# Performance work log

Measured on AMD Instinct MI355X. Metric: run time of the kernel, lower is better.

The kernel has to match this reference:

```python
import jax, jax.numpy as jnp
import numpy as np

B, C, F, H = 8, 256, 128, 256  # batch, channels(nodes), bn_features, hidden_size


def setup_inputs() -> dict:
    key = jax.random.key(0)
    k1, k2, k3, k4 = jax.random.split(key, 4)
    s1 = 1.0 / np.sqrt(2 * F)  # torch Linear default init scale
    s2 = 1.0 / np.sqrt(H)
    return {
        "xa": jax.random.normal(k1, (B, C, F), dtype=jnp.float32),
        "W1": jax.random.uniform(k2, (H, 2 * F), jnp.float32, -s1, s1),
        "b1": jax.random.uniform(k3, (H,), jnp.float32, -s1, s1),
        "w2": jax.random.uniform(k4, (H,), jnp.float32, -s2, s2),
        "b2": jnp.zeros((), jnp.float32),
    }


def reference(xa, W1, b1, w2, b2):
    # Linear over cat([x_i, x_j]) == x_i @ Wa^T + x_j @ Wb^T  (split first layer;
    # identical math to torch's concat+Linear, avoids the (B,C,C,2F) concat).
    f = xa.shape[-1]
    Wa, Wb = W1[:, :f], W1[:, f:]
    a = jnp.einsum('bif,hf->bih', xa, Wa)          # (B,C,H)
    c = jnp.einsum('bjf,hf->bjh', xa, Wb)          # (B,C,H)
    h = jax.nn.relu(a[:, :, None, :] + c[:, None, :, :] + b1)  # (B,C,C,H)
    edge_logits = jnp.einsum('bijh,h->bij', h, w2) + b2         # (B,C,C)
    return jax.nn.sigmoid(edge_logits)
```

## Files before the change

kernel.cpp:

```cpp
#include <hip/hip_runtime.h>


typedef _Float16 h2 __attribute__((ext_vector_type(2)));
typedef _Float16 h8 __attribute__((ext_vector_type(8)));
typedef float    f4 __attribute__((ext_vector_type(4)));

constexpr int B  = 8;
constexpr int C  = 256;
constexpr int F  = 128;
constexpr int H  = 256;
constexpr int F2 = 2 * F;
constexpr int HOCT = H / 8;

#if __has_builtin(__builtin_amdgcn_fdot2)
__device__ __forceinline__ float fdot2(h2 a, h2 b, float c) {
    return __builtin_amdgcn_fdot2(a, b, c, false);
}
#else
__device__ __forceinline__ float fdot2(h2 a, h2 b, float c) {
    return c + (float)a.x * (float)b.x + (float)a.y * (float)b.y;
}
#endif

__device__ __forceinline__ h8 cvt8(float4 a, float4 b) {
    h8 r;
    r[0] = (_Float16)a.x; r[1] = (_Float16)a.y; r[2] = (_Float16)a.z; r[3] = (_Float16)a.w;
    r[4] = (_Float16)b.x; r[5] = (_Float16)b.y; r[6] = (_Float16)b.z; r[7] = (_Float16)b.w;
    return r;
}

__global__ __launch_bounds__(256) void k1_mfma(
    const float* __restrict__ xa, const float* __restrict__ W1,
    const float* __restrict__ b1, const float* __restrict__ w2,
    _Float16* __restrict__ Ah, _Float16* __restrict__ CP8,
    _Float16* __restrict__ w2h)
{
    const int t  = threadIdx.x;
    const int w  = blockIdx.x * 4 + (t >> 6);
    const int l  = t & 63;
    const int mg = w >> 4;
    const int h0 = (w & 15) * 16;
    const int lm = l & 15;
    const int lk = (l >> 4) * 8;
    const int m0 = mg * 32;

    h8 af[2][4];
    const float* xp0 = xa + (size_t)(m0 + lm) * F + lk;
    const float* xp1 = xp0 + 16 * F;
    #pragma unroll
    for (int kk = 0; kk < 4; ++kk) {
        float4 a0 = *(const float4*)(xp0 + kk * 32);
        float4 a1 = *(const float4*)(xp0 + kk * 32 + 4);
        float4 b0 = *(const float4*)(xp1 + kk * 32);
        float4 b1v = *(const float4*)(xp1 + kk * 32 + 4);
        af[0][kk] = cvt8(a0, a1);
        af[1][kk] = cvt8(b0, b1v);
    }

    const float* wp = W1 + (size_t)(h0 + lm) * F2 + lk;
    f4 accA0 = {0.f,0.f,0.f,0.f}, accA1 = {0.f,0.f,0.f,0.f};
    f4 accC0 = {0.f,0.f,0.f,0.f}, accC1 = {0.f,0.f,0.f,0.f};
    #pragma unroll
    for (int kk = 0; kk < 4; ++kk) {
        float4 wa0 = *(const float4*)(wp + kk * 32);
        float4 wa1 = *(const float4*)(wp + kk * 32 + 4);
        float4 wb0 = *(const float4*)(wp + F + kk * 32);
        float4 wb1 = *(const float4*)(wp + F + kk * 32 + 4);
        h8 ba = cvt8(wa0, wa1);
        h8 bb = cvt8(wb0, wb1);
        accA0 = __builtin_amdgcn_mfma_f32_16x16x32_f16(af[0][kk], ba, accA0, 0, 0, 0);
        accC0 = __builtin_amdgcn_mfma_f32_16x16x32_f16(af[0][kk], bb, accC0, 0, 0, 0);
        accA1 = __builtin_amdgcn_mfma_f32_16x16x32_f16(af[1][kk], ba, accA1, 0, 0, 0);
        accC1 = __builtin_amdgcn_mfma_f32_16x16x32_f16(af[1][kk], bb, accC1, 0, 0, 0);
    }

    const int h  = h0 + lm;
    const float bh = b1[h];
    #pragma unroll
    for (int mt = 0; mt < 2; ++mt) {
        const f4 aA = mt ? accA1 : accA0;
        const f4 aC = mt ? accC1 : accC0;
        const int mb = m0 + mt * 16 + (l >> 4) * 4;
        #pragma unroll
        for (int r = 0; r < 4; ++r) {
            const int m = mb + r;
            Ah[(size_t)m * H + h] = (_Float16)(aA[r] + bh);
            CP8[(((size_t)((m >> 8) * HOCT + (h >> 3)) * C + (m & 255)) << 3) + (h & 7)]
                = (_Float16)aC[r];
        }
    }

    if (blockIdx.x == 0 && t < 128) {
        float2 wv = ((const float2*)w2)[t];
        h2 hv = {(_Float16)wv.x, (_Float16)wv.y};
        ((h2*)w2h)[t] = hv;
    }
}

constexpr int TI = 8;
constexpr int HS = 4;

__global__ __launch_bounds__(1024) void k2_pair(
    const _Float16* __restrict__ Ah, const _Float16* __restrict__ CP8,
    const _Float16* __restrict__ w2h, const float* __restrict__ b2p,
    float* __restrict__ out)
{
    __shared__ float red[(HS - 1) * TI * C];
    const int t   = threadIdx.x;
    const int j   = t & 255;
    const int hs  = t >> 8;
    const int blk = blockIdx.x;
    const int it  = blk & 31;
    const int b   = blk >> 5;
    const int i0  = it * TI;

    float acc[TI];
    #pragma unroll
    for (int ii = 0; ii < TI; ++ii) acc[ii] = 0.f;

    const int g0 = hs * (HOCT / HS);
    const _Float16* Ab = Ah + (size_t)(b * C + i0) * H;

    union U { h8 v; h2 p[4]; };
    #pragma unroll 2
    for (int g = 0; g < HOCT / HS; ++g) {
        const int hb = g0 + g;
        h8 cc = *(const h8*)(CP8 + (((size_t)(b * HOCT + hb) * C + j) << 3));
        U uw; uw.v = *(const h8*)(w2h + hb * 8);
        #pragma unroll
        for (int ii = 0; ii < TI; ++ii) {
            h8 av = *(const h8*)(Ab + ii * H + hb * 8);
            h8 s = av + cc;
            h8 z = {0, 0, 0, 0, 0, 0, 0, 0};
            s = __builtin_elementwise_max(s, z);
            U us; us.v = s;
            float a0 = acc[ii];
            a0 = fdot2(us.p[0], uw.p[0], a0);
            a0 = fdot2(us.p[1], uw.p[1], a0);
            a0 = fdot2(us.p[2], uw.p[2], a0);
            a0 = fdot2(us.p[3], uw.p[3], a0);
            acc[ii] = a0;
        }
    }

    if (hs > 0) {
        #pragma unroll
        for (int ii = 0; ii < TI; ++ii)
            red[((hs - 1) * TI + ii) * C + j] = acc[ii];
    }
    __syncthreads();
    if (hs == 0) {
        const float bb = b2p[0];
        #pragma unroll
        for (int ii = 0; ii < TI; ++ii) {
            float x = acc[ii]
                    + red[(0 * TI + ii) * C + j]
                    + red[(1 * TI + ii) * C + j]
                    + red[(2 * TI + ii) * C + j] + bb;
            out[(size_t)(b * C + i0 + ii) * C + j] = 1.f / (1.f + __expf(-x));
        }
    }
}

extern "C" void kernel_launch(void* const* d_in, const int* in_sizes, int n_in,
                              void* d_out, int out_size, void* d_ws, size_t ws_size,
                              hipStream_t stream) {
    const float* xa = (const float*)d_in[0];
    const float* W1 = (const float*)d_in[1];
    const float* b1 = (const float*)d_in[2];
    const float* w2 = (const float*)d_in[3];
    const float* b2 = (const float*)d_in[4];
    float* out = (float*)d_out;

    _Float16* Ah  = (_Float16*)d_ws;
    _Float16* CP8 = Ah  + (size_t)B * C * H;
    _Float16* w2h = CP8 + (size_t)B * H * C;

    k1_mfma<<<256, 256, 0, stream>>>(xa, W1, b1, w2, Ah, CP8, w2h);
    k2_pair<<<B * (C / TI), 1024, 0, stream>>>(Ah, CP8, w2h, b2, out);
}
```

Baseline: 23.84 us.

## Fuse projection and pair kernels into one cooperative launch with grid sync

Merges the MFMA projection kernel and the pairwise edge kernel into a single cooperative kernel of 256 blocks by 1024 threads. The first 256 threads of each block do the projection, then a grid-wide sync separates the two phases. w2 is now converted to fp16 straight into registers instead of going through workspace memory, and the hidden loop is fully unrolled. This removes one launch and the gap between kernels, but adds grid-sync overhead, leaves 3/4 of the threads idle during phase one, and raises register pressure.

Result: slower. 62.35 us (+161.5%).

```diff
diff --git a/kernel.cpp b/kernel.cpp
--- a/kernel.cpp
+++ b/kernel.cpp
@@ -1,4 +1,7 @@
 #include <hip/hip_runtime.h>
+#include <hip/hip_cooperative_groups.h>
+
+namespace cg = cooperative_groups;
 
 
 typedef _Float16 h2 __attribute__((ext_vector_type(2)));
@@ -11,6 +14,8 @@
 constexpr int H  = 256;
 constexpr int F2 = 2 * F;
 constexpr int HOCT = H / 8;
+constexpr int TI = 8;
+constexpr int HS = 4;
 
 #if __has_builtin(__builtin_amdgcn_fdot2)
 __device__ __forceinline__ float fdot2(h2 a, h2 b, float c) {
@@ -29,90 +34,83 @@
     return r;
 }
 
-__global__ __launch_bounds__(256) void k1_mfma(
+__global__ __launch_bounds__(1024) void fused_kernel(
     const float* __restrict__ xa, const float* __restrict__ W1,
     const float* __restrict__ b1, const float* __restrict__ w2,
-    _Float16* __restrict__ Ah, _Float16* __restrict__ CP8,
-    _Float16* __restrict__ w2h)
+    const float* __restrict__ b2p, float* __restrict__ out,
+    _Float16* __restrict__ Ah, _Float16* __restrict__ CP8)
 {
-    const int t  = threadIdx.x;
-    const int w  = blockIdx.x * 4 + (t >> 6);
-    const int l  = t & 63;
-    const int mg = w >> 4;
-    const int h0 = (w & 15) * 16;
-    const int lm = l & 15;
-    const int lk = (l >> 4) * 8;
-    const int m0 = mg * 32;
+    __shared__ float red[(HS - 1) * TI * C];
+    const int t   = threadIdx.x;
+    const int blk = blockIdx.x;
 
-    h8 af[2][4];
-    const float* xp0 = xa + (size_t)(m0 + lm) * F + lk;
-    const float* xp1 = xp0 + 16 * F;
-    #pragma unroll
-    for (int kk = 0; kk < 4; ++kk) {
-        float4 a0 = *(const float4*)(xp0 + kk * 32);
-        float4 a1 = *(const float4*)(xp0 + kk * 32 + 4);
-        float4 b0 = *(const float4*)(xp1 + kk * 32);
-        float4 b1v = *(const float4*)(xp1 + kk * 32 + 4);
-        af[0][kk] = cvt8(a0, a1);
-        af[1][kk] = cvt8(b0, b1v);
-    }
+    if (t < 256) {
+        const int w  = blk * 4 + (t >> 6);
+        const int l  = t & 63;
+        const int mg = w >> 4;
+        const int h0 = (w & 15) * 16;
+        const int lm = l & 15;
+        const int lk = (l >> 4) * 8;
+        const int m0 = mg * 32;
 
-    const float* wp = W1 + (size_t)(h0 + lm) * F2 + lk;
-    f4 accA0 = {0.f,0.f,0.f,0.f}, accA1 = {0.f,0.f,0.f,0.f};
-    f4 accC0 = {0.f,0.f,0.f,0.f}, accC1 = {0.f,0.f,0.f,0.f};
-    #pragma unroll
-    for (int kk = 0; kk < 4; ++kk) {
-        float4 wa0 = *(const float4*)(wp + kk * 32);
-        float4 wa1 = *(const float4*)(wp + kk * 32 + 4);
-        float4 wb0 = *(const float4*)(wp + F + kk * 32);
-        float4 wb1 = *(const float4*)(wp + F + kk * 32 + 4);
-        h8 ba = cvt8(wa0, wa1);
-        h8 bb = cvt8(wb0, wb1);
-        accA0 = __builtin_amdgcn_mfma_f32_16x16x32_f16(af[0][kk], ba, accA0, 0, 0, 0);
-        accC0 = __builtin_amdgcn_mfma_f32_16x16x32_f16(af[0][kk], bb, accC0, 0, 0, 0);
-        accA1 = __builtin_amdgcn_mfma_f32_16x16x32_f16(af[1][kk], ba, accA1, 0, 0, 0);
-        accC1 = __builtin_amdgcn_mfma_f32_16x16x32_f16(af[1][kk], bb, accC1, 0, 0, 0);
-    }
+        h8 af[2][4];
+        const float* xp0 = xa + (size_t)(m0 + lm) * F + lk;
+        const float* xp1 = xp0 + 16 * F;
+        #pragma unroll
+        for (int kk = 0; kk < 4; ++kk) {
+            af[0][kk] = cvt8(*(const float4*)(xp0 + kk * 32),
+                             *(const float4*)(xp0 + kk * 32 + 4));
+            af[1][kk] = cvt8(*(const float4*)(xp1 + kk * 32),
+                             *(const float4*)(xp1 + kk * 32 + 4));
+        }
 
-    const int h  = h0 + lm;
-    const float bh = b1[h];
-    #pragma unroll
-    for (int mt = 0; mt < 2; ++mt) {
-        const f4 aA = mt ? accA1 : accA0;
-        const f4 aC = mt ? accC1 : accC0;
-        const int mb = m0 + mt * 16 + (l >> 4) * 4;
+        const float* wp = W1 + (size_t)(h0 + lm) * F2 + lk;
+        f4 accA0 = {0.f,0.f,0.f,0.f}, accA1 = {0.f,0.f,0.f,0.f};
+        f4 accC0 = {0.f,0.f,0.f,0.f}, accC1 = {0.f,0.f,0.f,0.f};
         #pragma unroll
-        for (int r = 0; r < 4; ++r) {
-            const int m = mb + r;
-            Ah[(size_t)m * H + h] = (_Float16)(aA[r] + bh);
-            CP8[(((size_t)((m >> 8) * HOCT + (h >> 3)) * C + (m & 255)) << 3) + (h & 7)]
-                = (_Float16)aC[r];
+        for (int kk = 0; kk < 4; ++kk) {
+            h8 ba = cvt8(*(const float4*)(wp + kk * 32),
+                         *(const float4*)(wp + kk * 32 + 4));
+            h8 bb = cvt8(*(const float4*)(wp + F + kk * 32),
+                         *(const float4*)(wp + F + kk * 32 + 4));
+            accA0 = __builtin_amdgcn_mfma_f32_16x16x32_f16(af[0][kk], ba, accA0, 0, 0, 0);
+            accC0 = __builtin_amdgcn_mfma_f32_16x16x32_f16(af[0][kk], bb, accC0, 0, 0, 0);
+            accA1 = __builtin_amdgcn_mfma_f32_16x16x32_f16(af[1][kk], ba, accA1, 0, 0, 0);
+            accC1 = __builtin_amdgcn_mfma_f32_16x16x32_f16(af[1][kk], bb, accC1, 0, 0, 0);
+        }
+
+        const int h   = h0 + lm;
+        const float bh = b1[h];
+        #pragma unroll
+        for (int mt = 0; mt < 2; ++mt) {
+            const f4 aA = mt ? accA1 : accA0;
+            const f4 aC = mt ? accC1 : accC0;
+            const int mb = m0 + mt * 16 + (l >> 4) * 4;
+            #pragma unroll
+            for (int r = 0; r < 4; ++r) {
+                const int m = mb + r;
+                Ah[(size_t)m * H + h] = (_Float16)(aA[r] + bh);
+                CP8[(((size_t)((m >> 8) * HOCT + (h >> 3)) * C + (m & 255)) << 3) + (h & 7)]
+                    = (_Float16)aC[r];
+            }
         }
     }
 
-    if (blockIdx.x == 0 && t < 128) {
-        float2 wv = ((const float2*)w2)[t];
-        h2 hv = {(_Float16)wv.x, (_Float16)wv.y};
-        ((h2*)w2h)[t] = hv;
+    const int j  = t & 255;
+    const int hs = t >> 8;
+    h8 w2r[8];
+    {
+        const float4* wq = (const float4*)(w2 + hs * 64);
+        #pragma unroll
+        for (int o = 0; o < 8; ++o)
+            w2r[o] = cvt8(wq[2 * o], wq[2 * o + 1]);
     }
-}
 
-constexpr int TI = 8;
-constexpr int HS = 4;
+    cg::this_grid().sync();
 
-__global__ __launch_bounds__(1024) void k2_pair(
-    const _Float16* __restrict__ Ah, const _Float16* __restrict__ CP8,
-    const _Float16* __restrict__ w2h, const float* __restrict__ b2p,
-    float* __restrict__ out)
-{
-    __shared__ float red[(HS - 1) * TI * C];
-    const int t   = threadIdx.x;
-    const int j   = t & 255;
-    const int hs  = t >> 8;
-    const int blk = blockIdx.x;
-    const int it  = blk & 31;
-    const int b   = blk >> 5;
-    const int i0  = it * TI;
+    const int it = blk & 31;
+    const int b  = blk >> 5;
+    const int i0 = it * TI;
 
     float acc[TI];
     #pragma unroll
@@ -122,11 +120,11 @@
     const _Float16* Ab = Ah + (size_t)(b * C + i0) * H;
 
     union U { h8 v; h2 p[4]; };
-    #pragma unroll 2
+    #pragma unroll
     for (int g = 0; g < HOCT / HS; ++g) {
         const int hb = g0 + g;
         h8 cc = *(const h8*)(CP8 + (((size_t)(b * HOCT + hb) * C + j) << 3));
-        U uw; uw.v = *(const h8*)(w2h + hb * 8);
+        U uw; uw.v = w2r[g];
         #pragma unroll
         for (int ii = 0; ii < TI; ++ii) {
             h8 av = *(const h8*)(Ab + ii * H + hb * 8);
@@ -173,9 +171,10 @@
     float* out = (float*)d_out;
 
     _Float16* Ah  = (_Float16*)d_ws;
-    _Float16* CP8 = Ah  + (size_t)B * C * H;
-    _Float16* w2h = CP8 + (size_t)B * H * C;
+    _Float16* CP8 = Ah + (size_t)B * C * H;
 
-    k1_mfma<<<256, 256, 0, stream>>>(xa, W1, b1, w2, Ah, CP8, w2h);
-    k2_pair<<<B * (C / TI), 1024, 0, stream>>>(Ah, CP8, w2h, b2, out);
+    void* args[] = { (void*)&xa, (void*)&W1, (void*)&b1, (void*)&w2,
+                     (void*)&b2, (void*)&out, (void*)&Ah, (void*)&CP8 };
+    hipLaunchCooperativeKernel((void*)fused_kernel, dim3(256), dim3(1024),
+                               args, 0, stream);
 }
```

## Compute pairwise w2 reduction with MFMA instead of fdot2 and shared-memory reduce

Applied to the files above, without the earlier changes.

Rewrites the pair kernel so each wave takes 16 j-columns and runs the 256-long hidden reduction against w2 on 16x16x32 f16 MFMA. The relu(A+C) tile is the A operand and w2 is replicated across the B columns. This replaces the per-thread fdot2 chains, the four-way hidden split and the LDS cross-slice reduction with register accumulation, and writes output as float4. It wastes 15 of 16 MFMA output columns and keeps the packed add/max on VALU. Launch shape changes to 512 blocks of 512 threads.

After: 30.34 us. 1.27x slower.

```diff
diff --git a/kernel.cpp b/kernel.cpp
--- a/kernel.cpp
+++ b/kernel.cpp
@@ -11,16 +11,6 @@
 constexpr int H  = 256;
 constexpr int F2 = 2 * F;
 constexpr int HOCT = H / 8;
-
-#if __has_builtin(__builtin_amdgcn_fdot2)
-__device__ __forceinline__ float fdot2(h2 a, h2 b, float c) {
-    return __builtin_amdgcn_fdot2(a, b, c, false);
-}
-#else
-__device__ __forceinline__ float fdot2(h2 a, h2 b, float c) {
-    return c + (float)a.x * (float)b.x + (float)a.y * (float)b.y;
-}
-#endif
 
 __device__ __forceinline__ h8 cvt8(float4 a, float4 b) {
     h8 r;
@@ -49,12 +39,10 @@
     const float* xp1 = xp0 + 16 * F;
     #pragma unroll
     for (int kk = 0; kk < 4; ++kk) {
-        float4 a0 = *(const float4*)(xp0 + kk * 32);
-        float4 a1 = *(const float4*)(xp0 + kk * 32 + 4);
-        float4 b0 = *(const float4*)(xp1 + kk * 32);
-        float4 b1v = *(const float4*)(xp1 + kk * 32 + 4);
-        af[0][kk] = cvt8(a0, a1);
-        af[1][kk] = cvt8(b0, b1v);
+        af[0][kk] = cvt8(*(const float4*)(xp0 + kk * 32),
+                         *(const float4*)(xp0 + kk * 32 + 4));
+        af[1][kk] = cvt8(*(const float4*)(xp1 + kk * 32),
+                         *(const float4*)(xp1 + kk * 32 + 4));
     }
 
     const float* wp = W1 + (size_t)(h0 + lm) * F2 + lk;
@@ -62,12 +50,10 @@
     f4 accC0 = {0.f,0.f,0.f,0.f}, accC1 = {0.f,0.f,0.f,0.f};
     #pragma unroll
     for (int kk = 0; kk < 4; ++kk) {
-        float4 wa0 = *(const float4*)(wp + kk * 32);
-        float4 wa1 = *(const float4*)(wp + kk * 32 + 4);
-        float4 wb0 = *(const float4*)(wp + F + kk * 32);
-        float4 wb1 = *(const float4*)(wp + F + kk * 32 + 4);
-        h8 ba = cvt8(wa0, wa1);
-        h8 bb = cvt8(wb0, wb1);
+        h8 ba = cvt8(*(const float4*)(wp + kk * 32),
+                     *(const float4*)(wp + kk * 32 + 4));
+        h8 bb = cvt8(*(const float4*)(wp + F + kk * 32),
+                     *(const float4*)(wp + F + kk * 32 + 4));
         accA0 = __builtin_amdgcn_mfma_f32_16x16x32_f16(af[0][kk], ba, accA0, 0, 0, 0);
         accC0 = __builtin_amdgcn_mfma_f32_16x16x32_f16(af[0][kk], bb, accC0, 0, 0, 0);
         accA1 = __builtin_amdgcn_mfma_f32_16x16x32_f16(af[1][kk], ba, accA1, 0, 0, 0);
@@ -97,67 +83,59 @@
     }
 }
 
-constexpr int TI = 8;
-constexpr int HS = 4;
-
-__global__ __launch_bounds__(1024) void k2_pair(
+__global__ __launch_bounds__(512) void k2_mm(
     const _Float16* __restrict__ Ah, const _Float16* __restrict__ CP8,
     const _Float16* __restrict__ w2h, const float* __restrict__ b2p,
     float* __restrict__ out)
 {
-    __shared__ float red[(HS - 1) * TI * C];
-    const int t   = threadIdx.x;
-    const int j   = t & 255;
-    const int hs  = t >> 8;
-    const int blk = blockIdx.x;
-    const int it  = blk & 31;
-    const int b   = blk >> 5;
-    const int i0  = it * TI;
+    const int t    = threadIdx.x;
+    const int blk  = blockIdx.x;
+    const int jh   = blk & 1;
+    const int it   = (blk >> 1) & 31;
+    const int b    = blk >> 6;
+    const int i0   = it * 8;
+    const int w    = t >> 6;
+    const int l    = t & 63;
+    const int jrow = l & 15;
+    const int ks   = l >> 4;
+    const int j0   = (jh * 8 + w) * 16;
+    const int j    = j0 + jrow;
 
-    float acc[TI];
+    h8 ccf[8], w2f[8];
     #pragma unroll
-    for (int ii = 0; ii < TI; ++ii) acc[ii] = 0.f;
+    for (int s = 0; s < 8; ++s) {
+        const int hoct = 4 * s + ks;
+        ccf[s] = *(const h8*)(CP8 + (((size_t)(b * HOCT + hoct) * C + j) << 3));
+        w2f[s] = *(const h8*)(w2h + hoct * 8);
+    }
 
-    const int g0 = hs * (HOCT / HS);
-    const _Float16* Ab = Ah + (size_t)(b * C + i0) * H;
+    f4 acc[8];
+    #pragma unroll
+    for (int i = 0; i < 8; ++i) acc[i] = (f4){0.f, 0.f, 0.f, 0.f};
 
-    union U { h8 v; h2 p[4]; };
-    #pragma unroll 2
-    for (int g = 0; g < HOCT / HS; ++g) {
-        const int hb = g0 + g;
-        h8 cc = *(const h8*)(CP8 + (((size_t)(b * HOCT + hb) * C + j) << 3));
-        U uw; uw.v = *(const h8*)(w2h + hb * 8);
+    const _Float16* Ab = Ah + (size_t)(b * C + i0) * H + ks * 8;
+    const h8 z = {0, 0, 0, 0, 0, 0, 0, 0};
+    #pragma unroll
+    for (int s = 0; s < 8; ++s) {
         #pragma unroll
-        for (int ii = 0; ii < TI; ++ii) {
-            h8 av = *(const h8*)(Ab + ii * H + hb * 8);
-            h8 s = av + cc;
-            h8 z = {0, 0, 0, 0, 0, 0, 0, 0};
-            s = __builtin_elementwise_max(s, z);
-            U us; us.v = s;
-            float a0 = acc[ii];
-            a0 = fdot2(us.p[0], uw.p[0], a0);
-            a0 = fdot2(us.p[1], uw.p[1], a0);
-            a0 = fdot2(us.p[2], uw.p[2], a0);
-            a0 = fdot2(us.p[3], uw.p[3], a0);
-            acc[ii] = a0;
+        for (int i = 0; i < 8; ++i) {
+            h8 ao = *(const h8*)(Ab + (size_t)i * H + s * 32);
+            h8 sum = ao + ccf[s];
+            sum = __builtin_elementwise_max(sum, z);
+            acc[i] = __builtin_amdgcn_mfma_f32_16x16x32_f16(sum, w2f[s], acc[i], 0, 0, 0);
         }
     }
 
-    if (hs > 0) {
-        #pragma unroll
-        for (int ii = 0; ii < TI; ++ii)
-            red[((hs - 1) * TI + ii) * C + j] = acc[ii];
-    }
-    __syncthreads();
-    if (hs == 0) {
+    if (jrow == 0) {
         const float bb = b2p[0];
         #pragma unroll
-        for (int ii = 0; ii < TI; ++ii) {
-            float x = acc[ii]
-                    + red[(0 * TI + ii) * C + j]
-                    + red[(1 * TI + ii) * C + j]
-                    + red[(2 * TI + ii) * C + j] + bb;
-            out[(size_t)(b * C + i0 + ii) * C + j] = 1.f / (1.f + __expf(-x));
+        for (int i = 0; i < 8; ++i) {
+            float4 o;
+            o.x = 1.f / (1.f + __expf(-(acc[i][0] + bb)));
+            o.y = 1.f / (1.f + __expf(-(acc[i][1] + bb)));
+            o.z = 1.f / (1.f + __expf(-(acc[i][2] + bb)));
+            o.w = 1.f / (1.f + __expf(-(acc[i][3] + bb)));
+            *(float4*)(out + ((size_t)(b * C + i0 + i) * C + j0 + ks * 4)) = o;
         }
     }
 }
@@ -177,5 +155,5 @@
     _Float16* w2h = CP8 + (size_t)B * H * C;
 
     k1_mfma<<<256, 256, 0, stream>>>(xa, W1, b1, w2, Ah, CP8, w2h);
-    k2_pair<<<B * (C / TI), 1024, 0, stream>>>(Ah, CP8, w2h, b2, out);
+    k2_mm<<<512, 512, 0, stream>>>(Ah, CP8, w2h, b2, out);
 }
```
